# Kernel optimization log

Hardware: AMD Instinct MI355X
Metric: run time of the kernel (lower is better)

The kernel has to match this reference:

```python
import jax, jax.numpy as jnp
import numpy as np

B, T, C, H = 128, 256, 1024, 64


def setup_inputs() -> dict:
    key = jax.random.key(0)
    k1, k2, k3, k4 = jax.random.split(key, 4)
    # Glorot-ish scale for weights
    s = 1.0 / np.sqrt(C)
    return {
        "x": jax.random.normal(k1, (B, T, C), dtype=jnp.float32),
        "Wk": jax.random.normal(k2, (C, H), dtype=jnp.float32) * s,
        "Wq": jax.random.normal(k3, (C, H), dtype=jnp.float32) * s,
        "Wv": jax.random.normal(k4, (C, H), dtype=jnp.float32) * s,
    }


def reference(x, Wk, Wq, Wv):
    # Projections (no bias, matching use_bias=False)
    k = jnp.einsum("btc,ch->bth", x, Wk)  # [B,T,H]
    q = jnp.einsum("btc,ch->bth", x, Wq)
    v = jnp.einsum("btc,ch->bth", x, Wv)
    scale = k.shape[-1] ** -0.5
    wei = jnp.einsum("bth,bsh->bts", q, k) * scale  # [B,T,T]
    t = x.shape[1]
    causal = jnp.tril(jnp.ones((t, t), dtype=bool))
    wei = jnp.where(causal, wei, -jnp.inf)
    wei = jax.nn.softmax(wei, axis=-1)
    # dropout is identity at inference
    out = jnp.einsum("bts,bsh->bth", wei, v)  # [B,T,H]
    return out
```

## Files before the change

kernel.cpp:

```cpp
#include <hip/hip_runtime.h>
#include <hip/hip_bf16.h>

typedef __bf16 v8bf __attribute__((ext_vector_type(8)));
typedef float f32x16 __attribute__((ext_vector_type(16)));
typedef unsigned int uint;
typedef unsigned short ushort;

#define GLOAD16(gsrc, ldst)                                                       \
  __builtin_amdgcn_global_load_lds(                                               \
      (const __attribute__((address_space(1))) unsigned int*)(gsrc),              \
      (__attribute__((address_space(3))) unsigned int*)(ldst), 16, 0, 0)

__device__ inline f32x16 zero16() {
  f32x16 z;
#pragma unroll
  for (int i = 0; i < 16; i++) z[i] = 0.f;
  return z;
}

__device__ inline uint pack_bf16(float a, float b) {
  union { __bf16 h[2]; uint u; } c;
  c.h[0] = (__bf16)a;
  c.h[1] = (__bf16)b;
  return c.u;
}

__global__ void prep_wt(const float* __restrict__ Wq, const float* __restrict__ Wk,
                        const float* __restrict__ Wv, char* __restrict__ Wt_s) {
  __shared__ __bf16 tile[64][74];
  const int mat = blockIdx.x >> 4;
  const int c0 = (blockIdx.x & 15) * 64;
  const float* src = (mat == 0) ? Wq : (mat == 1) ? Wk : Wv;
  const int t = threadIdx.x;
  {
    const int r = t >> 2;
    const int ch = (t & 3) * 16;
    const float4* s4 = (const float4*)(src + (size_t)(c0 + r) * 64 + ch);
#pragma unroll
    for (int j = 0; j < 4; j++) {
      float4 f = s4[j];
      tile[r][ch + 4 * j + 0] = (__bf16)f.x;
      tile[r][ch + 4 * j + 1] = (__bf16)f.y;
      tile[r][ch + 4 * j + 2] = (__bf16)f.z;
      tile[r][ch + 4 * j + 3] = (__bf16)f.w;
    }
  }
  __syncthreads();
  const int h = t >> 2;
  const int cc = (t & 3) * 16;
  union { __bf16 o[16]; uint4 u[2]; } pk;
#pragma unroll
  for (int j = 0; j < 16; j++) pk.o[j] = tile[cc + j][h];
  const int n = mat * 64 + h;
  char* base = Wt_s + (size_t)n * 2048 + (c0 >> 6) * 128;
  const int bc = cc * 2;
  *(uint4*)(base + ((bc) ^ ((n & 7) << 4))) = pk.u[0];
  *(uint4*)(base + ((bc + 16) ^ ((n & 7) << 4))) = pk.u[1];
}

__launch_bounds__(256, 2)
__global__ void proj_kernel(const float* __restrict__ x, const char* __restrict__ Wt_s,
                            __bf16* __restrict__ KQV) {
  __shared__ char lds[65536];
  char* A0 = lds;
  char* A1 = lds + 8192;
  char* W0 = lds + 16384;
  char* W1 = lds + 40960;

  const int tid = threadIdx.x;
  const int lane = tid & 63;
  const int wave = tid >> 6;
  const int wm = wave >> 1;
  const int wn = wave & 1;
  const int row0 = blockIdx.x * 64;

  const int sr = tid >> 2;
  const int sc = tid & 3;
  const float4* xp = (const float4*)(x + (size_t)(row0 + sr) * 1024 + sc * 16);

  f32x16 acc[3];
#pragma unroll
  for (int i = 0; i < 3; i++) acc[i] = zero16();

  float4 rA[4], rB[4];

#define LOADA(rr, t)                                                              \
  {                                                                               \
    _Pragma("unroll") for (int j = 0; j < 4; j++) rr[j] = xp[(t) * 16 + j];       \
  }

#define GW(t, Wbuf)                                                               \
  {                                                                               \
    _Pragma("unroll") for (int j = 0; j < 6; j++) {                               \
      int idx = wave * 64 + j * 256 + lane;                                       \
      GLOAD16(Wt_s + (size_t)(idx >> 3) * 2048 + (t) * 128 + (idx & 7) * 16,      \
              Wbuf + wave * 1024 + j * 4096);                                     \
    }                                                                             \
  }

#define CVTWRITE(rr, Abuf)                                                        \
  {                                                                               \
    union { __bf16 h[16]; uint4 u[2]; } cv;                                       \
    _Pragma("unroll") for (int j = 0; j < 4; j++) {                               \
      cv.h[4 * j + 0] = (__bf16)rr[j].x;                                          \
      cv.h[4 * j + 1] = (__bf16)rr[j].y;                                          \
      cv.h[4 * j + 2] = (__bf16)rr[j].z;                                          \
      cv.h[4 * j + 3] = (__bf16)rr[j].w;                                          \
    }                                                                             \
    *(uint4*)(Abuf + sr * 128 + ((sc * 32) ^ ((sr & 7) << 4))) = cv.u[0];         \
    *(uint4*)(Abuf + sr * 128 + ((sc * 32 + 16) ^ ((sr & 7) << 4))) = cv.u[1];    \
  }

#define MMA(Abuf, Wbuf)                                                           \
  {                                                                               \
    _Pragma("unroll") for (int ks = 0; ks < 4; ks++) {                            \
      int arow = wm * 32 + (lane & 31);                                           \
      int kb = ks * 32 + ((lane >> 5) << 4);                                      \
      v8bf av = *(const v8bf*)(Abuf + arow * 128 + (kb ^ ((arow & 7) << 4)));     \
      _Pragma("unroll") for (int nf = 0; nf < 3; nf++) {                          \
        int brow = wn * 96 + nf * 32 + (lane & 31);                               \
        v8bf bv = *(const v8bf*)(Wbuf + brow * 128 + (kb ^ ((brow & 7) << 4)));   \
        acc[nf] = __builtin_amdgcn_mfma_f32_32x32x16_bf16(av, bv, acc[nf], 0, 0, 0); \
      }                                                                           \
    }                                                                             \
  }

  GW(0, W0);
  LOADA(rA, 0);
  CVTWRITE(rA, A0);
  __syncthreads();

  for (int t = 0; t < 16; t += 2) {
    GW(t + 1, W1);
    LOADA(rB, t + 1);
    __builtin_amdgcn_sched_barrier(0);
    MMA(A0, W0);
    CVTWRITE(rB, A1);
    __syncthreads();
    if (t + 2 < 16) {
      GW(t + 2, W0);
      LOADA(rA, t + 2);
    }
    __builtin_amdgcn_sched_barrier(0);
    MMA(A1, W1);
    if (t + 2 < 16) {
      CVTWRITE(rA, A0);
      __syncthreads();
    }
  }

#pragma unroll
  for (int nf = 0; nf < 3; nf++) {
#pragma unroll
    for (int r = 0; r < 16; r++) {
      int row = row0 + wm * 32 + (r & 3) + ((r >> 2) << 3) + ((lane >> 5) << 2);
      int col = wn * 96 + nf * 32 + (lane & 31);
      KQV[(size_t)row * 192 + col] = (__bf16)acc[nf][r];
    }
  }
#undef LOADA
#undef GW
#undef CVTWRITE
#undef MMA
}

__launch_bounds__(256, 1)
__global__ void attn_kernel(const __bf16* __restrict__ KQV, float* __restrict__ out) {
  __shared__ uint4 lds4[81920 / 16];
  char* Klds = (char*)lds4;
  char* Vlds = (char*)lds4 + 32768;
  char* Qlds = (char*)lds4 + 65536;

  const int tid = threadIdx.x;
  const int lane = tid & 63;
  const int wave = tid >> 6;
  const int b = blockIdx.x >> 1;
  const int half = blockIdx.x & 1;
  const int bt0 = half * 128;
  const size_t base = (size_t)b * 256 * 192;

  {
    int s = tid;
    const uint4* src = (const uint4*)(KQV + base + (size_t)s * 192 + 64);
#pragma unroll
    for (int i = 0; i < 8; i++) {
      uint4 v = src[i];
      int byte = s * 128 + ((i * 16) ^ ((s & 7) << 4));
      *(uint4*)(Klds + byte) = v;
    }
  }
  {
    int s = tid;
    const uint4* src = (const uint4*)(KQV + base + (size_t)s * 192 + 128);
#pragma unroll
    for (int i = 0; i < 8; i++) {
      uint4 v = src[i];
      const ushort* e = (const ushort*)&v;
#pragma unroll
      for (int j = 0; j < 8; j++) {
        int h = i * 8 + j;
        int byte = h * 512 + ((s * 2) ^ ((h & 7) << 4));
        *(ushort*)(Vlds + byte) = e[j];
      }
    }
  }
#pragma unroll
  for (int i = 0; i < 4; i++) {
    int c = tid + i * 256;
    int r = c >> 3, cc = c & 7;
    uint4 v = *(const uint4*)(KQV + base + (size_t)(bt0 + r) * 192 + cc * 8);
    int byte = r * 128 + ((cc * 16) ^ ((r & 7) << 4));
    *(uint4*)(Qlds + byte) = v;
  }
  __syncthreads();

  const int t0 = bt0 + wave * 32;
  const int tg = t0 + (lane & 31);
  const int nf = (t0 >> 5) + 1;

  f32x16 sacc[8];
#pragma unroll
  for (int sf = 0; sf < 8; sf++) {
    f32x16 sv = zero16();
    if (sf < nf) {
#pragma unroll
      for (int ks = 0; ks < 4; ks++) {
        int kbyte = ks * 32 + ((lane >> 5) << 4);
        int krow = sf * 32 + (lane & 31);
        v8bf a = *(const v8bf*)(Klds + krow * 128 + (kbyte ^ ((krow & 7) << 4)));
        int qrow = wave * 32 + (lane & 31);
        v8bf bq = *(const v8bf*)(Qlds + qrow * 128 + (kbyte ^ ((qrow & 7) << 4)));
        sv = __builtin_amdgcn_mfma_f32_32x32x16_bf16(a, bq, sv, 0, 0, 0);
      }
    }
    sacc[sf] = sv;
  }

  float m = -1e30f;
#pragma unroll
  for (int sf = 0; sf < 8; sf++) {
    if (sf < nf) {
#pragma unroll
      for (int r = 0; r < 16; r++) {
        int sg = sf * 32 + (r & 3) + ((r >> 2) << 3) + ((lane >> 5) << 2);
        float v = sacc[sf][r] * 0.125f;
        v = (sg > tg) ? -1e30f : v;
        sacc[sf][r] = v;
        m = fmaxf(m, v);
      }
    }
  }
  m = fmaxf(m, __shfl_xor(m, 32, 64));
  float l = 0.f;
#pragma unroll
  for (int sf = 0; sf < 8; sf++) {
    if (sf < nf) {
#pragma unroll
      for (int r = 0; r < 16; r++) {
        float p = __expf(sacc[sf][r] - m);
        sacc[sf][r] = p;
        l += p;
      }
    }
  }
  l += __shfl_xor(l, 32, 64);
  float inv = 1.0f / l;

  f32x16 oacc[2];
  oacc[0] = zero16();
  oacc[1] = zero16();
  const bool hiLane = (lane >= 32);
#pragma unroll
  for (int sf = 0; sf < 8; sf++) {
    if (sf < nf) {
      uint w[8], ow[8];
#pragma unroll
      for (int q = 0; q < 4; q++) {
        w[2 * q]     = pack_bf16(sacc[sf][4 * q] * inv,     sacc[sf][4 * q + 1] * inv);
        w[2 * q + 1] = pack_bf16(sacc[sf][4 * q + 2] * inv, sacc[sf][4 * q + 3] * inv);
      }
#pragma unroll
      for (int i = 0; i < 8; i++) ow[i] = (uint)__shfl_xor((int)w[i], 32, 64);
#pragma unroll
      for (int ks = 0; ks < 2; ks++) {
        int bse = 4 * ks;
        union { uint u[4]; v8bf v; } A;
        A.u[0] = hiLane ? ow[bse + 2] : w[bse + 0];
        A.u[1] = hiLane ? ow[bse + 3] : w[bse + 1];
        A.u[2] = hiLane ? w[bse + 2] : ow[bse + 0];
        A.u[3] = hiLane ? w[bse + 3] : ow[bse + 1];
        int sbyte0 = (sf * 32 + ks * 16) * 2 + ((lane >> 5) << 4);
#pragma unroll
        for (int hf = 0; hf < 2; hf++) {
          int vrow = hf * 32 + (lane & 31);
          v8bf bv = *(const v8bf*)(Vlds + vrow * 512 + (sbyte0 ^ ((vrow & 7) << 4)));
          oacc[hf] = __builtin_amdgcn_mfma_f32_32x32x16_bf16(A.v, bv, oacc[hf], 0, 0, 0);
        }
      }
    }
  }

#pragma unroll
  for (int hf = 0; hf < 2; hf++) {
#pragma unroll
    for (int r = 0; r < 16; r++) {
      int t = t0 + (r & 3) + ((r >> 2) << 3) + ((lane >> 5) << 2);
      int h = hf * 32 + (lane & 31);
      out[((size_t)b * 256 + t) * 64 + h] = oacc[hf][r];
    }
  }
}

extern "C" void kernel_launch(void* const* d_in, const int* in_sizes, int n_in,
                              void* d_out, int out_size, void* d_ws, size_t ws_size,
                              hipStream_t stream) {
  const float* x  = (const float*)d_in[0];
  const float* Wk = (const float*)d_in[1];
  const float* Wq = (const float*)d_in[2];
  const float* Wv = (const float*)d_in[3];
  float* out = (float*)d_out;

  __bf16* KQV = (__bf16*)d_ws;
  char* Wt_s  = (char*)d_ws + (size_t)32768 * 192 * 2;

  prep_wt<<<48, 256, 0, stream>>>(Wq, Wk, Wv, Wt_s);
  proj_kernel<<<512, 256, 0, stream>>>(x, Wt_s, KQV);
  attn_kernel<<<256, 256, 0, stream>>>(KQV, out);
}
```

Baseline: 46.74 us.

## Load fp32 activations directly into LDS and convert to bf16 at MMA time

The projection kernel now streams fp32 x tiles straight into LDS with global_load_lds (using an XOR swizzle) instead of staging them through registers, converting and writing bf16. Each wave converts fp32 to bf16 while reading its MMA operands, and the sched barriers are removed, which simplifies the pipeline. The intent is to cut register pressure and VALU/LDS-write work in the main loop and let the A loads proceed asynchronously. In exchange, the LDS footprint grows to 80KB, which may limit the two-blocks-per-CU target, and the conversion work is repeated across the two wn waves that share each A row.

```diff
diff --git a/kernel.cpp b/kernel.cpp
--- a/kernel.cpp
+++ b/kernel.cpp
@@ -61,11 +61,11 @@
 __launch_bounds__(256, 2)
 __global__ void proj_kernel(const float* __restrict__ x, const char* __restrict__ Wt_s,
                             __bf16* __restrict__ KQV) {
-  __shared__ char lds[65536];
+  __shared__ char lds[81920];
   char* A0 = lds;
-  char* A1 = lds + 8192;
-  char* W0 = lds + 16384;
-  char* W1 = lds + 40960;
+  char* A1 = lds + 16384;
+  char* W0 = lds + 32768;
+  char* W1 = lds + 57344;
 
   const int tid = threadIdx.x;
   const int lane = tid & 63;
@@ -74,19 +74,22 @@
   const int wn = wave & 1;
   const int row0 = blockIdx.x * 64;
 
-  const int sr = tid >> 2;
-  const int sc = tid & 3;
-  const float4* xp = (const float4*)(x + (size_t)(row0 + sr) * 1024 + sc * 16);
+  const int sL = wave * 64 + lane;
+  const int sr = sL >> 4;
+  const int ss = sL & 15;
 
   f32x16 acc[3];
 #pragma unroll
   for (int i = 0; i < 3; i++) acc[i] = zero16();
 
-  float4 rA[4], rB[4];
-
-#define LOADA(rr, t)                                                              \
+#define GA(t, Abuf)                                                               \
   {                                                                               \
-    _Pragma("unroll") for (int j = 0; j < 4; j++) rr[j] = xp[(t) * 16 + j];       \
+    _Pragma("unroll") for (int i = 0; i < 4; i++) {                               \
+      int r = sr + i * 16;                                                        \
+      int c4 = ss ^ (r & 15);                                                     \
+      GLOAD16(x + (size_t)(row0 + r) * 1024 + (t) * 64 + c4 * 4,                  \
+              Abuf + wave * 1024 + i * 4096);                                     \
+    }                                                                             \
   }
 
 #define GW(t, Wbuf)                                                               \
@@ -98,55 +101,45 @@
     }                                                                             \
   }
 
-#define CVTWRITE(rr, Abuf)                                                        \
-  {                                                                               \
-    union { __bf16 h[16]; uint4 u[2]; } cv;                                       \
-    _Pragma("unroll") for (int j = 0; j < 4; j++) {                               \
-      cv.h[4 * j + 0] = (__bf16)rr[j].x;                                          \
-      cv.h[4 * j + 1] = (__bf16)rr[j].y;                                          \
-      cv.h[4 * j + 2] = (__bf16)rr[j].z;                                          \
-      cv.h[4 * j + 3] = (__bf16)rr[j].w;                                          \
-    }                                                                             \
-    *(uint4*)(Abuf + sr * 128 + ((sc * 32) ^ ((sr & 7) << 4))) = cv.u[0];         \
-    *(uint4*)(Abuf + sr * 128 + ((sc * 32 + 16) ^ ((sr & 7) << 4))) = cv.u[1];    \
-  }
-
 #define MMA(Abuf, Wbuf)                                                           \
   {                                                                               \
     _Pragma("unroll") for (int ks = 0; ks < 4; ks++) {                            \
       int arow = wm * 32 + (lane & 31);                                           \
-      int kb = ks * 32 + ((lane >> 5) << 4);                                      \
-      v8bf av = *(const v8bf*)(Abuf + arow * 128 + (kb ^ ((arow & 7) << 4)));     \
+      int hi = lane >> 5;                                                         \
+      int c4 = ks * 4 + hi * 2;                                                   \
+      float4 f0 = *(const float4*)(Abuf + arow * 256 +                            \
+                                   ((c4 * 16) ^ ((arow & 15) << 4)));             \
+      float4 f1 = *(const float4*)(Abuf + arow * 256 +                            \
+                                   (((c4 + 1) * 16) ^ ((arow & 15) << 4)));       \
+      union { __bf16 h[8]; v8bf v; } av;                                          \
+      av.h[0] = (__bf16)f0.x; av.h[1] = (__bf16)f0.y;                             \
+      av.h[2] = (__bf16)f0.z; av.h[3] = (__bf16)f0.w;                             \
+      av.h[4] = (__bf16)f1.x; av.h[5] = (__bf16)f1.y;                             \
+      av.h[6] = (__bf16)f1.z; av.h[7] = (__bf16)f1.w;                             \
+      int kb = ks * 32 + (hi << 4);                                               \
       _Pragma("unroll") for (int nf = 0; nf < 3; nf++) {                          \
         int brow = wn * 96 + nf * 32 + (lane & 31);                               \
         v8bf bv = *(const v8bf*)(Wbuf + brow * 128 + (kb ^ ((brow & 7) << 4)));   \
-        acc[nf] = __builtin_amdgcn_mfma_f32_32x32x16_bf16(av, bv, acc[nf], 0, 0, 0); \
+        acc[nf] = __builtin_amdgcn_mfma_f32_32x32x16_bf16(av.v, bv, acc[nf], 0, 0, 0); \
       }                                                                           \
     }                                                                             \
   }
 
+  GA(0, A0);
   GW(0, W0);
-  LOADA(rA, 0);
-  CVTWRITE(rA, A0);
   __syncthreads();
 
   for (int t = 0; t < 16; t += 2) {
+    GA(t + 1, A1);
     GW(t + 1, W1);
-    LOADA(rB, t + 1);
-    __builtin_amdgcn_sched_barrier(0);
     MMA(A0, W0);
-    CVTWRITE(rB, A1);
     __syncthreads();
     if (t + 2 < 16) {
+      GA(t + 2, A0);
       GW(t + 2, W0);
-      LOADA(rA, t + 2);
-    }
-    __builtin_amdgcn_sched_barrier(0);
+    }
     MMA(A1, W1);
-    if (t + 2 < 16) {
-      CVTWRITE(rA, A0);
-      __syncthreads();
-    }
+    __syncthreads();
   }
 
 #pragma unroll
@@ -158,9 +151,8 @@
       KQV[(size_t)row * 192 + col] = (__bf16)acc[nf][r];
     }
   }
-#undef LOADA
+#undef GA
 #undef GW
-#undef CVTWRITE
 #undef MMA
 }
 
```

Result: slower. 51.65 us (+10.5%).

## Deepen projection GEMM pipeline with two-ahead register prefetch and partial vmcnt waits

Applied to the files above, without the earlier changes.

Restructures the QKV projection main loop into a fully unrolled pipeline that prefetches x tiles two steps ahead into four rotating register sets, and keeps the W tile one step ahead via global_load_lds. __syncthreads is replaced by an explicit s_waitcnt vmcnt(4) plus s_barrier, so the most recent global loads can stay in flight across the barrier. The aim is to hide global memory latency behind the MFMA work. In exchange it uses more registers, and the correctness of the partial vmcnt count depends on the order in which loads are issued.

```diff
diff --git a/kernel.cpp b/kernel.cpp
--- a/kernel.cpp
+++ b/kernel.cpp
@@ -82,7 +82,9 @@
 #pragma unroll
   for (int i = 0; i < 3; i++) acc[i] = zero16();
 
-  float4 rA[4], rB[4];
+  float4 s0[4], s1[4], s2[4], s3[4];
+
+#define SB __builtin_amdgcn_sched_barrier(0)
 
 #define LOADA(rr, t)                                                              \
   {                                                                               \
@@ -125,29 +127,56 @@
     }                                                                             \
   }
 
+#define BAR4                                                                      \
+  do {                                                                            \
+    asm volatile("s_waitcnt vmcnt(4) lgkmcnt(0)" ::: "memory");                   \
+    __builtin_amdgcn_s_barrier();                                                 \
+    SB;                                                                           \
+  } while (0)
+#define BAR0                                                                      \
+  do {                                                                            \
+    asm volatile("s_waitcnt vmcnt(0) lgkmcnt(0)" ::: "memory");                   \
+    __builtin_amdgcn_s_barrier();                                                 \
+    SB;                                                                           \
+  } while (0)
+
+#define STEP(T, SI, SC_, ACUR, WCUR, ANXT, WNXT)                                  \
+  GW(T + 1, WNXT);                                                                \
+  SB;                                                                             \
+  LOADA(SI, T + 2);                                                               \
+  SB;                                                                             \
+  MMA(ACUR, WCUR);                                                                \
+  CVTWRITE(SC_, ANXT);                                                            \
+  BAR4;
+
   GW(0, W0);
-  LOADA(rA, 0);
-  CVTWRITE(rA, A0);
-  __syncthreads();
-
-  for (int t = 0; t < 16; t += 2) {
-    GW(t + 1, W1);
-    LOADA(rB, t + 1);
-    __builtin_amdgcn_sched_barrier(0);
-    MMA(A0, W0);
-    CVTWRITE(rB, A1);
-    __syncthreads();
-    if (t + 2 < 16) {
-      GW(t + 2, W0);
-      LOADA(rA, t + 2);
-    }
-    __builtin_amdgcn_sched_barrier(0);
-    MMA(A1, W1);
-    if (t + 2 < 16) {
-      CVTWRITE(rA, A0);
-      __syncthreads();
-    }
-  }
+  SB;
+  LOADA(s0, 0);
+  LOADA(s1, 1);
+  SB;
+  CVTWRITE(s0, A0);
+  BAR4;
+
+  STEP(0, s2, s1, A0, W0, A1, W1)
+  STEP(1, s3, s2, A1, W1, A0, W0)
+  STEP(2, s0, s3, A0, W0, A1, W1)
+  STEP(3, s1, s0, A1, W1, A0, W0)
+  STEP(4, s2, s1, A0, W0, A1, W1)
+  STEP(5, s3, s2, A1, W1, A0, W0)
+  STEP(6, s0, s3, A0, W0, A1, W1)
+  STEP(7, s1, s0, A1, W1, A0, W0)
+  STEP(8, s2, s1, A0, W0, A1, W1)
+  STEP(9, s3, s2, A1, W1, A0, W0)
+  STEP(10, s0, s3, A0, W0, A1, W1)
+  STEP(11, s1, s0, A1, W1, A0, W0)
+  STEP(12, s2, s1, A0, W0, A1, W1)
+  STEP(13, s3, s2, A1, W1, A0, W0)
+  GW(15, W1);
+  SB;
+  MMA(A0, W0);
+  CVTWRITE(s3, A1);
+  BAR0;
+  MMA(A1, W1);
 
 #pragma unroll
   for (int nf = 0; nf < 3; nf++) {
@@ -158,10 +187,14 @@
       KQV[(size_t)row * 192 + col] = (__bf16)acc[nf][r];
     }
   }
+#undef STEP
+#undef BAR4
+#undef BAR0
 #undef LOADA
 #undef GW
 #undef CVTWRITE
 #undef MMA
+#undef SB
 }
 
 __launch_bounds__(256, 1)
```

New measurement: 45.67 us. -2.3%, faster.

## Load projection weights directly into registers in MFMA fragment layout

Applied to the files above, without the earlier changes.

The prep kernel now writes the bf16 weights pre-arranged in MFMA B-fragment order, so each wave reads its 12 weight fragments per k-tile straight from global memory (L2-resident) into registers, with no LDS staging. LDS use in the projection kernel drops to the double-buffered x tile, which removes the weight LDS traffic and may allow higher occupancy. The x loads are also prefetched two tiles ahead using four register sets, with a lighter barrier that only waits on LDS counters. The cost is more VGPR pressure and weight loads whose latency is no longer hidden through LDS.

```diff
diff --git a/kernel.cpp b/kernel.cpp
--- a/kernel.cpp
+++ b/kernel.cpp
@@ -5,11 +5,6 @@
 typedef float f32x16 __attribute__((ext_vector_type(16)));
 typedef unsigned int uint;
 typedef unsigned short ushort;
-
-#define GLOAD16(gsrc, ldst)                                                       \
-  __builtin_amdgcn_global_load_lds(                                               \
-      (const __attribute__((address_space(1))) unsigned int*)(gsrc),              \
-      (__attribute__((address_space(3))) unsigned int*)(ldst), 16, 0, 0)
 
 __device__ inline f32x16 zero16() {
   f32x16 z;
@@ -26,16 +21,16 @@
 }
 
 __global__ void prep_wt(const float* __restrict__ Wq, const float* __restrict__ Wk,
-                        const float* __restrict__ Wv, char* __restrict__ Wt_s) {
+                        const float* __restrict__ Wv, char* __restrict__ Wf) {
   __shared__ __bf16 tile[64][74];
   const int mat = blockIdx.x >> 4;
-  const int c0 = (blockIdx.x & 15) * 64;
+  const int kt = blockIdx.x & 15;
   const float* src = (mat == 0) ? Wq : (mat == 1) ? Wk : Wv;
-  const int t = threadIdx.x;
+  const int th = threadIdx.x;
   {
-    const int r = t >> 2;
-    const int ch = (t & 3) * 16;
-    const float4* s4 = (const float4*)(src + (size_t)(c0 + r) * 64 + ch);
+    const int r = th >> 2;
+    const int ch = (th & 3) * 16;
+    const float4* s4 = (const float4*)(src + (size_t)(kt * 64 + r) * 64 + ch);
 #pragma unroll
     for (int j = 0; j < 4; j++) {
       float4 f = s4[j];
@@ -46,26 +41,26 @@
     }
   }
   __syncthreads();
-  const int h = t >> 2;
-  const int cc = (t & 3) * 16;
+  const int h = th >> 2;
+  const int cc = (th & 3) * 16;
   union { __bf16 o[16]; uint4 u[2]; } pk;
 #pragma unroll
   for (int j = 0; j < 16; j++) pk.o[j] = tile[cc + j][h];
   const int n = mat * 64 + h;
-  char* base = Wt_s + (size_t)n * 2048 + (c0 >> 6) * 128;
-  const int bc = cc * 2;
-  *(uint4*)(base + ((bc) ^ ((n & 7) << 4))) = pk.u[0];
-  *(uint4*)(base + ((bc + 16) ^ ((n & 7) << 4))) = pk.u[1];
+  const int wn = (n >= 96) ? 1 : 0;
+  const int within = n - wn * 96;
+  const int nf = within >> 5;
+  const int c = within & 31;
+  const int ks = cc >> 4;
+  const size_t fb = (size_t)((((kt * 2 + wn) * 3 + nf) * 4) + ks) * 1024;
+  *(uint4*)(Wf + fb + c * 16) = pk.u[0];
+  *(uint4*)(Wf + fb + (32 + c) * 16) = pk.u[1];
 }
 
 __launch_bounds__(256, 2)
-__global__ void proj_kernel(const float* __restrict__ x, const char* __restrict__ Wt_s,
+__global__ void proj_kernel(const float* __restrict__ x, const char* __restrict__ Wf,
                             __bf16* __restrict__ KQV) {
-  __shared__ char lds[65536];
-  char* A0 = lds;
-  char* A1 = lds + 8192;
-  char* W0 = lds + 16384;
-  char* W1 = lds + 40960;
+  __shared__ char Alds[2][8192];
 
   const int tid = threadIdx.x;
   const int lane = tid & 63;
@@ -77,28 +72,27 @@
   const int sr = tid >> 2;
   const int sc = tid & 3;
   const float4* xp = (const float4*)(x + (size_t)(row0 + sr) * 1024 + sc * 16);
+  const char* wbase = Wf + (size_t)wn * 12288 + lane * 16;
 
   f32x16 acc[3];
 #pragma unroll
   for (int i = 0; i < 3; i++) acc[i] = zero16();
 
-  float4 rA[4], rB[4];
-
-#define LOADA(rr, t)                                                              \
+  float4 s0[4], s1[4], s2[4], s3[4];
+  v8bf wf[12];
+
+#define LOADA(rr, T)                                                              \
   {                                                                               \
-    _Pragma("unroll") for (int j = 0; j < 4; j++) rr[j] = xp[(t) * 16 + j];       \
-  }
-
-#define GW(t, Wbuf)                                                               \
+    _Pragma("unroll") for (int j = 0; j < 4; j++) rr[j] = xp[(T) * 16 + j];       \
+  }
+
+#define LOADW(T)                                                                  \
   {                                                                               \
-    _Pragma("unroll") for (int j = 0; j < 6; j++) {                               \
-      int idx = wave * 64 + j * 256 + lane;                                       \
-      GLOAD16(Wt_s + (size_t)(idx >> 3) * 2048 + (t) * 128 + (idx & 7) * 16,      \
-              Wbuf + wave * 1024 + j * 4096);                                     \
-    }                                                                             \
-  }
-
-#define CVTWRITE(rr, Abuf)                                                        \
+    _Pragma("unroll") for (int f = 0; f < 12; f++)                                \
+      wf[f] = *(const v8bf*)(wbase + (size_t)(T) * 24576 + f * 1024);             \
+  }
+
+#define CVTWRITE(rr, P)                                                           \
   {                                                                               \
     union { __bf16 h[16]; uint4 u[2]; } cv;                                       \
     _Pragma("unroll") for (int j = 0; j < 4; j++) {                               \
@@ -107,47 +101,62 @@
       cv.h[4 * j + 2] = (__bf16)rr[j].z;                                          \
       cv.h[4 * j + 3] = (__bf16)rr[j].w;                                          \
     }                                                                             \
-    *(uint4*)(Abuf + sr * 128 + ((sc * 32) ^ ((sr & 7) << 4))) = cv.u[0];         \
-    *(uint4*)(Abuf + sr * 128 + ((sc * 32 + 16) ^ ((sr & 7) << 4))) = cv.u[1];    \
-  }
-
-#define MMA(Abuf, Wbuf)                                                           \
+    *(uint4*)(Alds[P] + sr * 128 + ((sc * 32) ^ ((sr & 7) << 4))) = cv.u[0];      \
+    *(uint4*)(Alds[P] + sr * 128 + ((sc * 32 + 16) ^ ((sr & 7) << 4))) = cv.u[1]; \
+  }
+
+#define MMA(P)                                                                    \
   {                                                                               \
     _Pragma("unroll") for (int ks = 0; ks < 4; ks++) {                            \
       int arow = wm * 32 + (lane & 31);                                           \
       int kb = ks * 32 + ((lane >> 5) << 4);                                      \
-      v8bf av = *(const v8bf*)(Abuf + arow * 128 + (kb ^ ((arow & 7) << 4)));     \
-      _Pragma("unroll") for (int nf = 0; nf < 3; nf++) {                          \
-        int brow = wn * 96 + nf * 32 + (lane & 31);                               \
-        v8bf bv = *(const v8bf*)(Wbuf + brow * 128 + (kb ^ ((brow & 7) << 4)));   \
-        acc[nf] = __builtin_amdgcn_mfma_f32_32x32x16_bf16(av, bv, acc[nf], 0, 0, 0); \
-      }                                                                           \
+      v8bf av = *(const v8bf*)(Alds[P] + arow * 128 + (kb ^ ((arow & 7) << 4)));  \
+      _Pragma("unroll") for (int nf = 0; nf < 3; nf++)                            \
+        acc[nf] = __builtin_amdgcn_mfma_f32_32x32x16_bf16(av, wf[nf * 4 + ks],    \
+                                                          acc[nf], 0, 0, 0);      \
     }                                                                             \
   }
 
-  GW(0, W0);
-  LOADA(rA, 0);
-  CVTWRITE(rA, A0);
-  __syncthreads();
-
-  for (int t = 0; t < 16; t += 2) {
-    GW(t + 1, W1);
-    LOADA(rB, t + 1);
-    __builtin_amdgcn_sched_barrier(0);
-    MMA(A0, W0);
-    CVTWRITE(rB, A1);
-    __syncthreads();
-    if (t + 2 < 16) {
-      GW(t + 2, W0);
-      LOADA(rA, t + 2);
-    }
-    __builtin_amdgcn_sched_barrier(0);
-    MMA(A1, W1);
-    if (t + 2 < 16) {
-      CVTWRITE(rA, A0);
-      __syncthreads();
-    }
-  }
+#define LBAR                                                                      \
+  do {                                                                            \
+    asm volatile("s_waitcnt lgkmcnt(0)" ::: "memory");                            \
+    __builtin_amdgcn_s_barrier();                                                 \
+  } while (0)
+
+#define STEP(T, SN2, SN1)                                                         \
+  LOADW(T);                                                                       \
+  LOADA(SN2, (T) + 2);                                                            \
+  CVTWRITE(SN1, ((T) + 1) & 1);                                                   \
+  MMA((T) & 1);                                                                   \
+  LBAR;
+#define STEPL(T, SN1)                                        \
+  LOADW(T);                                                                       \
+  CVTWRITE(SN1, ((T) + 1) & 1);                                                   \
+  MMA((T) & 1);                                                                   \
+  LBAR;
+
+  LOADA(s0, 0);
+  LOADA(s1, 1);
+  CVTWRITE(s0, 0);
+  LBAR;
+
+  STEP(0, s2, s1)
+  STEP(1, s3, s2)
+  STEP(2, s0, s3)
+  STEP(3, s1, s0)
+  STEP(4, s2, s1)
+  STEP(5, s3, s2)
+  STEP(6, s0, s3)
+  STEP(7, s1, s0)
+  STEP(8, s2, s1)
+  STEP(9, s3, s2)
+  STEP(10, s0, s3)
+  STEP(11, s1, s0)
+  STEP(12, s2, s1)
+  STEP(13, s3, s2)
+  STEPL(14, s3)
+  LOADW(15);
+  MMA(1);
 
 #pragma unroll
   for (int nf = 0; nf < 3; nf++) {
@@ -158,8 +167,11 @@
       KQV[(size_t)row * 192 + col] = (__bf16)acc[nf][r];
     }
   }
+#undef STEP
+#undef STEPL
+#undef LBAR
 #undef LOADA
-#undef GW
+#undef LOADW
 #undef CVTWRITE
 #undef MMA
 }
@@ -321,9 +333,9 @@
   float* out = (float*)d_out;
 
   __bf16* KQV = (__bf16*)d_ws;
-  char* Wt_s  = (char*)d_ws + (size_t)32768 * 192 * 2;
-
-  prep_wt<<<48, 256, 0, stream>>>(Wq, Wk, Wv, Wt_s);
-  proj_kernel<<<512, 256, 0, stream>>>(x, Wt_s, KQV);
+  char* Wf = (char*)d_ws + (size_t)32768 * 192 * 2;
+
+  prep_wt<<<48, 256, 0, stream>>>(Wq, Wk, Wv, Wf);
+  proj_kernel<<<512, 256, 0, stream>>>(x, Wf, KQV);
   attn_kernel<<<256, 256, 0, stream>>>(KQV, out);
 }
```

After: 61.36 us. 31.3% more time.
